# Performance work log

Measured on AMD Instinct MI355X. Metric: run time of the kernel, lower is better.

The kernel has to match this reference:

```python
import jax, jax.numpy as jnp
import numpy as np

INPUT, HIDDEN, OUTPUT = 512, 1024, 512
B, T = 64, 512


def setup_inputs() -> dict:
    key = jax.random.key(0)
    ks = jax.random.split(key, 10)
    s_ih = (2.0 / (INPUT + HIDDEN)) ** 0.5
    s_hh = (2.0 / (INPUT + HIDDEN)) ** 0.5
    s_hy = (2.0 / (HIDDEN + OUTPUT)) ** 0.5
    inp = {
        "x": jax.random.normal(ks[0], (B, T, INPUT), dtype=jnp.float32),
        "W_xi": jax.random.normal(ks[1], (INPUT, HIDDEN), dtype=jnp.float32) * s_ih,
        "W_hi": jax.random.normal(ks[2], (HIDDEN, HIDDEN), dtype=jnp.float32) * s_hh,
        "b_i": jnp.zeros((HIDDEN,), dtype=jnp.float32),
        "W_xf": jax.random.normal(ks[3], (INPUT, HIDDEN), dtype=jnp.float32) * s_ih,
        "W_hf": jax.random.normal(ks[4], (HIDDEN, HIDDEN), dtype=jnp.float32) * s_hh,
        "b_f": jnp.zeros((HIDDEN,), dtype=jnp.float32),
        "W_xo": jax.random.normal(ks[5], (INPUT, HIDDEN), dtype=jnp.float32) * s_ih,
        "W_ho": jax.random.normal(ks[6], (HIDDEN, HIDDEN), dtype=jnp.float32) * s_hh,
        "b_o": jnp.zeros((HIDDEN,), dtype=jnp.float32),
        "W_xc": jax.random.normal(ks[7], (INPUT, HIDDEN), dtype=jnp.float32) * s_ih,
        "W_hc": jax.random.normal(ks[8], (HIDDEN, HIDDEN), dtype=jnp.float32) * s_hh,
        "b_c": jnp.zeros((HIDDEN,), dtype=jnp.float32),
        "W_hy": jax.random.normal(ks[9], (HIDDEN, OUTPUT), dtype=jnp.float32) * s_hy,
        "b_y": jnp.zeros((OUTPUT,), dtype=jnp.float32),
    }
    return inp


def reference(x, W_xi, W_hi, b_i, W_xf, W_hf, b_f, W_xo, W_ho, b_o,
              W_xc, W_hc, b_c, W_hy, b_y):
    Bn, Tn, _ = x.shape
    H = W_hi.shape[0]
    # Precompute input projections for all timesteps (one big GEMM per gate).
    xi = jnp.einsum('bti,ih->bth', x, W_xi) + b_i  # [B,T,H]
    xf = jnp.einsum('bti,ih->bth', x, W_xf) + b_f
    xo = jnp.einsum('bti,ih->bth', x, W_xo) + b_o
    xc = jnp.einsum('bti,ih->bth', x, W_xc) + b_c
    # time-major for scan
    xs = (jnp.swapaxes(xi, 0, 1), jnp.swapaxes(xf, 0, 1),
          jnp.swapaxes(xo, 0, 1), jnp.swapaxes(xc, 0, 1))

    def step(carry, xt):
        h, c = carry
        xi_t, xf_t, xo_t, xc_t = xt
        i_t = jax.nn.sigmoid(xi_t + h @ W_hi)
        f_t = jax.nn.sigmoid(xf_t + h @ W_hf)
        o_t = jax.nn.sigmoid(xo_t + h @ W_ho)
        cand = jnp.tanh(xc_t + h @ W_hc)
        c = f_t * c + i_t * cand
        h = o_t * jnp.tanh(c)
        return (h, c), h

    h0 = jnp.zeros((Bn, H), dtype=x.dtype)
    c0 = jnp.zeros((Bn, H), dtype=x.dtype)
    _, hs = jax.lax.scan(step, (h0, c0), xs)  # hs: [T,B,H]
    # Output projection applied to every step's hidden state.
    ys = jnp.einsum('tbh,ho->tbo', hs, W_hy) + b_y
    return jnp.swapaxes(ys, 0, 1)  # [B,T,O]
```

## Files before the change

kernel.cpp:

```cpp
#include <hip/hip_runtime.h>
#include <hip/hip_bf16.h>
#include <cstdint>

#define B_   64
#define T_   512
#define IN_  512
#define H_   1024
#define O_   512
#define NG   4096
#define KC   1536
#define BT   32768
#define BH   65536
#define NWG  256

#define GLB __attribute__((address_space(1)))
#define LDSAS __attribute__((address_space(3)))

using bs8 = __attribute__((ext_vector_type(8))) short;
using f4  = __attribute__((ext_vector_type(4))) float;
using u32x4 = __attribute__((ext_vector_type(4))) unsigned int;

__device__ __forceinline__ ushort f2bf(float f) {
    union { float f; uint32_t u; } v; v.f = f;
    uint32_t r = v.u + 0x7fffu + ((v.u >> 16) & 1u);
    return (ushort)(r >> 16);
}
__device__ __forceinline__ float sigm(float x) { return 1.f / (1.f + __expf(-x)); }
__device__ __forceinline__ float tanh_(float x) {
    x = fminf(fmaxf(x, -15.f), 15.f);
    float e = __expf(2.f * x);
    return (e - 1.f) / (e + 1.f);
}


__global__ void k_pack_x(const float* __restrict__ x, ushort* __restrict__ xP) {
    const int n8 = BT * IN_ / 8;
    for (int i = blockIdx.x * blockDim.x + threadIdx.x; i < n8; i += gridDim.x * blockDim.x) {
        const int e8 = i & 3, b = (i >> 2) & 63, kk = (i >> 8) & 15, t = i >> 12;
        const float* s = x + ((size_t)b * T_ + t) * IN_ + kk * 32 + e8 * 8;
        f4 v0 = *reinterpret_cast<const f4*>(s);
        f4 v1 = *reinterpret_cast<const f4*>(s + 4);
        uint4 q;
        q.x = (uint32_t)f2bf(v0[0]) | ((uint32_t)f2bf(v0[1]) << 16);
        q.y = (uint32_t)f2bf(v0[2]) | ((uint32_t)f2bf(v0[3]) << 16);
        q.z = (uint32_t)f2bf(v1[0]) | ((uint32_t)f2bf(v1[1]) << 16);
        q.w = (uint32_t)f2bf(v1[2]) | ((uint32_t)f2bf(v1[3]) << 16);
        *reinterpret_cast<uint4*>(xP + ((size_t)t * 16 + kk) * 2048 + b * 32 + e8 * 8) = q;
    }
}

__global__ void k_build_wcT(const float* __restrict__ xi, const float* __restrict__ xf,
                            const float* __restrict__ xo, const float* __restrict__ xc,
                            const float* __restrict__ hi, const float* __restrict__ hf,
                            const float* __restrict__ ho, const float* __restrict__ hc,
                            ushort* __restrict__ dst) {
    const int total = NG * KC;
    for (int i = blockIdx.x * blockDim.x + threadIdx.x; i < total; i += gridDim.x * blockDim.x) {
        int n = i / KC, k = i - n * KC;
        int g = n & 3, h = n >> 2;
        float v;
        if (k < IN_) {
            const float* s = (g == 0) ? xi : ((g == 1) ? xf : ((g == 2) ? xo : xc));
            v = s[(size_t)k * H_ + h];
        } else {
            const float* s = (g == 0) ? hi : ((g == 1) ? hf : ((g == 2) ? ho : hc));
            v = s[(size_t)(k - IN_) * H_ + h];
        }
        dst[i] = f2bf(v);
    }
}

__global__ void k_build_whyT(const float* __restrict__ w, ushort* __restrict__ dst) {
    const int total = O_ * H_;
    for (int i = blockIdx.x * blockDim.x + threadIdx.x; i < total; i += gridDim.x * blockDim.x) {
        int o = i >> 10, k = i & (H_ - 1);
        dst[i] = f2bf(w[(size_t)k * O_ + o]);
    }
}

__global__ void k_build_bias(const float* __restrict__ bi, const float* __restrict__ bff,
                             const float* __restrict__ bo, const float* __restrict__ bc,
                             float* __restrict__ dst) {
    int i = blockIdx.x * blockDim.x + threadIdx.x;
    if (i < NG) {
        int g = i & 3, h = i >> 2;
        dst[i] = (g == 0) ? bi[h] : ((g == 1) ? bff[h] : ((g == 2) ? bo[h] : bc[h]));
    }
}

__global__ void __launch_bounds__(256) __attribute__((amdgpu_waves_per_eu(1, 1)))
k_persist(const ushort* __restrict__ WcT, const ushort* __restrict__ xP,
          ushort* __restrict__ hs, float* __restrict__ cst,
          const float* __restrict__ biasc, uint32_t* __restrict__ flags,
          int t0, int nsteps) {
    __shared__ char Hst[4][32][1024];
    __shared__ ushort hout[64][4];
    const int g = blockIdx.x, tid = threadIdx.x;
    const int lane = tid & 63, w = tid >> 6;
    const int n0 = g * 16;
    const int l15 = lane & 15, lq = lane >> 4;

    bs8 wf[48];
#pragma unroll
    for (int c = 0; c < 48; ++c)
        wf[c] = *reinterpret_cast<const bs8*>(WcT + (size_t)(n0 + l15) * KC + c * 32 + lq * 8);

    const int bmy = w * 16 + l15;
    const int u = g * 4 + lq;
    const f4 bia = *reinterpret_cast<const f4*>(biasc + n0 + lq * 4);
    float creg = (t0 == 0) ? 0.f : cst[(size_t)bmy * H_ + u];

    const int lgo = ((lane >> 3) * 512) + (w * 128) + ((lane & 7) * 16);
    const char* hsb = (const char*)hs;
    const ushort* xb = xP + (size_t)bmy * 32 + lq * 8;
    const int lro = ((l15 >> 1) * 16) + ((l15 & 1) * 8);

    bs8 xv[16];
#pragma unroll
    for (int c = 0; c < 16; ++c)
        xv[c] = *reinterpret_cast<const bs8*>(xb + ((size_t)t0 * 16 + c) * 2048);

    __syncthreads();

    f4 acc[4];
    auto hcons = [&](int c) {
        const char* base = &Hst[w][c][0] + lro;
        union { bs8 v; uint2 p[2]; } uu;
        uu.p[0] = *reinterpret_cast<const uint2*>(base + (lq * 2 + 0) * 128);
        uu.p[1] = *reinterpret_cast<const uint2*>(base + (lq * 2 + 1) * 128);
        acc[c & 3] = __builtin_amdgcn_mfma_f32_16x16x32_bf16(wf[16 + c], uu.v, acc[c & 3], 0, 0, 0);
    };

    for (int s = 0; s < nsteps; ++s) {
        const char* slot = hsb + (size_t)s * 131072 + lgo;
#pragma unroll
        for (int c = 0; c < 32; ++c)
            __builtin_amdgcn_global_load_lds((const GLB uint32_t*)(slot + c * 4096),
                                             (LDSAS uint32_t*)(&Hst[w][c][0]), 16, 0, 0);

#pragma unroll
        for (int c = 0; c < 4; ++c) acc[c] = (f4){0.f, 0.f, 0.f, 0.f};
#pragma unroll
        for (int c = 0; c < 16; ++c)
            acc[c & 3] = __builtin_amdgcn_mfma_f32_16x16x32_bf16(wf[c], xv[c], acc[c & 3], 0, 0, 0);

        asm volatile("s_waitcnt vmcnt(24)" ::: "memory");
        __builtin_amdgcn_sched_barrier(0);
#pragma unroll
        for (int j = 0; j < 8; ++j) hcons(j);
        asm volatile("s_waitcnt vmcnt(16)" ::: "memory");
        __builtin_amdgcn_sched_barrier(0);
#pragma unroll
        for (int j = 8; j < 16; ++j) hcons(j);
        asm volatile("s_waitcnt vmcnt(8)" ::: "memory");
        __builtin_amdgcn_sched_barrier(0);
#pragma unroll
        for (int j = 16; j < 24; ++j) hcons(j);
        asm volatile("s_waitcnt vmcnt(0)" ::: "memory");
        __builtin_amdgcn_sched_barrier(0);
#pragma unroll
        for (int j = 24; j < 32; ++j) hcons(j);

        f4 ssum = (acc[0] + acc[1]) + (acc[2] + acc[3]);

        {
            float pi = ssum[0] + bia[0], pf = ssum[1] + bia[1];
            float po = ssum[2] + bia[2], pc = ssum[3] + bia[3];
            float iv = sigm(pi), fv = sigm(pf), ov = sigm(po), cv = tanh_(pc);
            creg = fv * creg + iv * cv;
            hout[bmy][lq] = f2bf(ov * tanh_(creg));
        }
        __syncthreads();

        if (w == 0) {
            uint2 hv2 = *reinterpret_cast<uint2*>(&hout[lane][0]);
            char* dst = (char*)hs + (size_t)(s + 1) * 131072 + (size_t)g * 512 + lane * 8;
            asm volatile("global_store_dwordx2 %0, %1, off sc0 sc1" :: "v"(dst), "v"(hv2) : "memory");
            asm volatile("s_waitcnt vmcnt(0)" ::: "memory");
            if (tid == 0)
                __hip_atomic_store(&flags[g], (uint32_t)(s + 1),
                                   __ATOMIC_RELAXED, __HIP_MEMORY_SCOPE_AGENT);
        }

        if (s + 1 < nsteps) {
#pragma unroll
            for (int c = 0; c < 16; ++c)
                xv[c] = *reinterpret_cast<const bs8*>(xb + ((size_t)(t0 + s + 1) * 16 + c) * 2048);
            if (w == 0) {
                const uint32_t tgt = (uint32_t)(s + 1);
                const uint32_t* fp = flags + lane * 4;
                for (;;) {
                    u32x4 f;
                    asm volatile("global_load_dwordx4 %0, %1, off sc0 sc1\n\t"
                                 "s_waitcnt vmcnt(0)"
                                 : "=v"(f) : "v"(fp) : "memory");
                    if (__all((int)(f.x >= tgt && f.y >= tgt && f.z >= tgt && f.w >= tgt))) break;
                    __builtin_amdgcn_s_sleep(1);
                }
            }
            __syncthreads();
        }
    }

    cst[(size_t)bmy * H_ + u] = creg;
}

__global__ void __launch_bounds__(64) k_yproj(const ushort* __restrict__ WhyT,
                                              const ushort* __restrict__ hsbase,
                                              const float* __restrict__ by,
                                              float* __restrict__ out, int t_off) {
    const int lane = threadIdx.x;
    const int tloc = blockIdx.x;
    const int o0 = blockIdx.y * 64;
    const int l15 = lane & 15, lq = lane >> 4, lk = lq * 8;
    const int t = t_off + tloc;

    const char* slot = (const char*)(hsbase + (size_t)(tloc + 1) * BH);
    const ushort* apm[4];
#pragma unroll
    for (int m = 0; m < 4; ++m) apm[m] = WhyT + (size_t)(o0 + m * 16 + l15) * H_ + lk;

    f4 acc[4][4] = {};
    for (int kk = 0; kk < 32; ++kk) {
        bs8 a[4], b[4];
#pragma unroll
        for (int m = 0; m < 4; ++m) a[m] = *reinterpret_cast<const bs8*>(apm[m] + kk * 32);
#pragma unroll
        for (int n = 0; n < 4; ++n) {
            const int bb = n * 16 + l15;
            union { bs8 v; uint2 p[2]; } uu;
            uu.p[0] = *reinterpret_cast<const uint2*>(slot + (size_t)(kk * 8 + lq * 2 + 0) * 512 + bb * 8);
            uu.p[1] = *reinterpret_cast<const uint2*>(slot + (size_t)(kk * 8 + lq * 2 + 1) * 512 + bb * 8);
            b[n] = uu.v;
        }
#pragma unroll
        for (int m = 0; m < 4; ++m)
#pragma unroll
            for (int n = 0; n < 4; ++n)
                acc[m][n] = __builtin_amdgcn_mfma_f32_16x16x32_bf16(a[m], b[n], acc[m][n], 0, 0, 0);
    }

#pragma unroll
    for (int m = 0; m < 4; ++m) {
        const int ob = o0 + m * 16 + lq * 4;
        const f4 bb = *reinterpret_cast<const f4*>(by + ob);
#pragma unroll
        for (int n = 0; n < 4; ++n) {
            const int b_ = n * 16 + l15;
            f4 v = acc[m][n] + bb;
            *reinterpret_cast<f4*>(out + ((size_t)b_ * T_ + t) * O_ + ob) = v;
        }
    }
}


extern "C" void kernel_launch(void* const* d_in, const int* in_sizes, int n_in,
                              void* d_out, int out_size, void* d_ws, size_t ws_size,
                              hipStream_t stream) {
    const float* x   = (const float*)d_in[0];
    const float* wxi = (const float*)d_in[1];
    const float* whi = (const float*)d_in[2];
    const float* bi  = (const float*)d_in[3];
    const float* wxf = (const float*)d_in[4];
    const float* whf = (const float*)d_in[5];
    const float* bf_ = (const float*)d_in[6];
    const float* wxo = (const float*)d_in[7];
    const float* who = (const float*)d_in[8];
    const float* bo  = (const float*)d_in[9];
    const float* wxc = (const float*)d_in[10];
    const float* whc = (const float*)d_in[11];
    const float* bc  = (const float*)d_in[12];
    const float* why = (const float*)d_in[13];
    const float* by  = (const float*)d_in[14];
    float* out = (float*)d_out;

    uint8_t* w = (uint8_t*)d_ws;
    ushort*   xP    = (ushort*)  (w);
    ushort*   WcT   = (ushort*)  (w + 33554432);
    ushort*   WhyT  = (ushort*)  (w + 46137344);
    float*    biasc = (float*)   (w + 47185920);
    float*    cst   = (float*)   (w + 47202304);
    uint32_t* flags = (uint32_t*)(w + 47464448);
    ushort*   hs    = (ushort*)  (w + 47468544);
    const size_t NEED_A = 47468544 + (size_t)(T_ + 1) * BH * 2;
    const size_t NEED_B = 47468544 + (size_t)65 * BH * 2;
    if (ws_size < NEED_B) return;
    const bool fullhs = (ws_size >= NEED_A);

    k_pack_x<<<2048, 256, 0, stream>>>(x, xP);
    k_build_wcT<<<4096, 256, 0, stream>>>(wxi, wxf, wxo, wxc, whi, whf, who, whc, WcT);
    k_build_whyT<<<512, 256, 0, stream>>>(why, WhyT);
    k_build_bias<<<16, 256, 0, stream>>>(bi, bf_, bo, bc, biasc);

    hipMemsetAsync(cst, 0, (size_t)BH * 4, stream);
    hipMemsetAsync(hs,  0, (size_t)BH * 2, stream);

    const int nchunk = fullhs ? 1 : 8;
    const int steps  = fullhs ? T_ : 64;
    for (int c = 0; c < nchunk; ++c) {
        const int t0 = c * steps;
        hipMemsetAsync(flags, 0, NWG * 4, stream);
        const ushort* a0 = WcT; const ushort* a1 = xP; ushort* a2 = hs;
        float* a3 = cst; const float* a4 = biasc; uint32_t* a5 = flags;
        int a6 = t0, a7 = steps;
        void* args[8] = {&a0, &a1, &a2, &a3, &a4, &a5, &a6, &a7};
        hipError_t e = hipLaunchCooperativeKernel((const void*)k_persist,
                                                  dim3(NWG), dim3(256), args, 0, stream);
        if (e != hipSuccess) {
            k_persist<<<dim3(NWG), dim3(256), 0, stream>>>(WcT, xP, hs, cst, biasc,
                                                           flags, t0, steps);
        }
        if (!fullhs) {
            k_yproj<<<dim3(64, O_ / 64), 64, 0, stream>>>(WhyT, hs, by, out, t0);
            if (c != nchunk - 1)
                hipMemcpyAsync(hs, hs + (size_t)64 * BH, (size_t)BH * 2,
                               hipMemcpyDeviceToDevice, stream);
        }
    }
    if (fullhs)
        k_yproj<<<dim3(T_, O_ / 64), 64, 0, stream>>>(WhyT, hs, by, out, 0);
}
```

Before: 2.695 ms.

## Split recurrent K across waves and overlap input-projection MFMAs with flag wait

Each wave now owns a quarter of the K-chunks for all 64 batch rows instead of the full K for 16 rows. Per-wave weight registers drop from 48 to 12 fragments, and the partial sums are reduced across waves through an LDS buffer. The input-projection MFMAs for the next step are issued before the flag poll, and the flag store no longer waits for all outstanding loads, so less of that work sits on the serial critical path. In exchange this adds an extra LDS reduction and barrier, and every wave now polls the flags without a trailing block barrier, which risks races on the shared buffers.

```diff
diff --git a/kernel.cpp b/kernel.cpp
--- a/kernel.cpp
+++ b/kernel.cpp
@@ -94,74 +94,91 @@
           const float* __restrict__ biasc, uint32_t* __restrict__ flags,
           int t0, int nsteps) {
     __shared__ char Hst[4][32][1024];
+    __shared__ f4 part[4][4][64];
     __shared__ ushort hout[64][4];
     const int g = blockIdx.x, tid = threadIdx.x;
     const int lane = tid & 63, w = tid >> 6;
     const int n0 = g * 16;
     const int l15 = lane & 15, lq = lane >> 4;
 
-    bs8 wf[48];
-#pragma unroll
-    for (int c = 0; c < 48; ++c)
-        wf[c] = *reinterpret_cast<const bs8*>(WcT + (size_t)(n0 + l15) * KC + c * 32 + lq * 8);
+    bs8 wf[12];
+#pragma unroll
+    for (int i = 0; i < 4; ++i)
+        wf[i] = *reinterpret_cast<const bs8*>(WcT + (size_t)(n0 + l15) * KC + (w + 4 * i) * 32 + lq * 8);
+#pragma unroll
+    for (int i = 0; i < 8; ++i)
+        wf[4 + i] = *reinterpret_cast<const bs8*>(WcT + (size_t)(n0 + l15) * KC + 512 + (w + 4 * i) * 32 + lq * 8);
 
     const int bmy = w * 16 + l15;
     const int u = g * 4 + lq;
     const f4 bia = *reinterpret_cast<const f4*>(biasc + n0 + lq * 4);
     float creg = (t0 == 0) ? 0.f : cst[(size_t)bmy * H_ + u];
 
-    const int lgo = ((lane >> 3) * 512) + (w * 128) + ((lane & 7) * 16);
     const char* hsb = (const char*)hs;
-    const ushort* xb = xP + (size_t)bmy * 32 + lq * 8;
+    const int lsg = ((lane >> 3) << 9) + ((lane & 7) << 4);
     const int lro = ((l15 >> 1) * 16) + ((l15 & 1) * 8);
 
     bs8 xv[16];
 #pragma unroll
-    for (int c = 0; c < 16; ++c)
-        xv[c] = *reinterpret_cast<const bs8*>(xb + ((size_t)t0 * 16 + c) * 2048);
+    for (int i = 0; i < 4; ++i)
+#pragma unroll
+        for (int bt = 0; bt < 4; ++bt)
+            xv[i * 4 + bt] = *reinterpret_cast<const bs8*>(
+                xP + ((size_t)t0 * 16 + (w + 4 * i)) * 2048 + (bt * 16 + l15) * 32 + lq * 8);
+    f4 acc[4];
+#pragma unroll
+    for (int bt = 0; bt < 4; ++bt) acc[bt] = (f4){0.f, 0.f, 0.f, 0.f};
+#pragma unroll
+    for (int i = 0; i < 4; ++i)
+#pragma unroll
+        for (int bt = 0; bt < 4; ++bt)
+            acc[bt] = __builtin_amdgcn_mfma_f32_16x16x32_bf16(wf[i], xv[i * 4 + bt], acc[bt], 0, 0, 0);
 
     __syncthreads();
 
-    f4 acc[4];
-    auto hcons = [&](int c) {
-        const char* base = &Hst[w][c][0] + lro;
+    auto hcons = [&](int i, int bt) {
+        const char* base = &Hst[w][i * 4 + bt][0] + lro;
         union { bs8 v; uint2 p[2]; } uu;
         uu.p[0] = *reinterpret_cast<const uint2*>(base + (lq * 2 + 0) * 128);
         uu.p[1] = *reinterpret_cast<const uint2*>(base + (lq * 2 + 1) * 128);
-        acc[c & 3] = __builtin_amdgcn_mfma_f32_16x16x32_bf16(wf[16 + c], uu.v, acc[c & 3], 0, 0, 0);
+        acc[bt] = __builtin_amdgcn_mfma_f32_16x16x32_bf16(wf[4 + i], uu.v, acc[bt], 0, 0, 0);
     };
 
     for (int s = 0; s < nsteps; ++s) {
-        const char* slot = hsb + (size_t)s * 131072 + lgo;
-#pragma unroll
-        for (int c = 0; c < 32; ++c)
-            __builtin_amdgcn_global_load_lds((const GLB uint32_t*)(slot + c * 4096),
-                                             (LDSAS uint32_t*)(&Hst[w][c][0]), 16, 0, 0);
-
-#pragma unroll
-        for (int c = 0; c < 4; ++c) acc[c] = (f4){0.f, 0.f, 0.f, 0.f};
-#pragma unroll
-        for (int c = 0; c < 16; ++c)
-            acc[c & 3] = __builtin_amdgcn_mfma_f32_16x16x32_bf16(wf[c], xv[c], acc[c & 3], 0, 0, 0);
+        {
+            const char* slot = hsb + (size_t)s * 131072;
+#pragma unroll
+            for (int i = 0; i < 8; ++i) {
+                const int hc = w + 4 * i;
+                const char* csrc = slot + (size_t)hc * 4096 + lsg;
+#pragma unroll
+                for (int bt = 0; bt < 4; ++bt)
+                    __builtin_amdgcn_global_load_lds((const GLB uint32_t*)(csrc + bt * 128),
+                                                     (LDSAS uint32_t*)(&Hst[w][i * 4 + bt][0]), 16, 0, 0);
+            }
+        }
 
         asm volatile("s_waitcnt vmcnt(24)" ::: "memory");
         __builtin_amdgcn_sched_barrier(0);
 #pragma unroll
-        for (int j = 0; j < 8; ++j) hcons(j);
+        for (int i = 0; i < 2; ++i) { hcons(i, 0); hcons(i, 1); hcons(i, 2); hcons(i, 3); }
         asm volatile("s_waitcnt vmcnt(16)" ::: "memory");
         __builtin_amdgcn_sched_barrier(0);
 #pragma unroll
-        for (int j = 8; j < 16; ++j) hcons(j);
+        for (int i = 2; i < 4; ++i) { hcons(i, 0); hcons(i, 1); hcons(i, 2); hcons(i, 3); }
         asm volatile("s_waitcnt vmcnt(8)" ::: "memory");
         __builtin_amdgcn_sched_barrier(0);
 #pragma unroll
-        for (int j = 16; j < 24; ++j) hcons(j);
+        for (int i = 4; i < 6; ++i) { hcons(i, 0); hcons(i, 1); hcons(i, 2); hcons(i, 3); }
         asm volatile("s_waitcnt vmcnt(0)" ::: "memory");
         __builtin_amdgcn_sched_barrier(0);
 #pragma unroll
-        for (int j = 24; j < 32; ++j) hcons(j);
-
-        f4 ssum = (acc[0] + acc[1]) + (acc[2] + acc[3]);
+        for (int i = 6; i < 8; ++i) { hcons(i, 0); hcons(i, 1); hcons(i, 2); hcons(i, 3); }
+
+#pragma unroll
+        for (int bt = 0; bt < 4; ++bt) part[w][bt][lane] = acc[bt];
+        __syncthreads();
+        f4 ssum = (part[0][w][lane] + part[1][w][lane]) + (part[2][w][lane] + part[3][w][lane]);
 
         {
             float pi = ssum[0] + bia[0], pf = ssum[1] + bia[1];
@@ -176,17 +193,29 @@
             uint2 hv2 = *reinterpret_cast<uint2*>(&hout[lane][0]);
             char* dst = (char*)hs + (size_t)(s + 1) * 131072 + (size_t)g * 512 + lane * 8;
             asm volatile("global_store_dwordx2 %0, %1, off sc0 sc1" :: "v"(dst), "v"(hv2) : "memory");
-            asm volatile("s_waitcnt vmcnt(0)" ::: "memory");
-            if (tid == 0)
-                __hip_atomic_store(&flags[g], (uint32_t)(s + 1),
-                                   __ATOMIC_RELAXED, __HIP_MEMORY_SCOPE_AGENT);
         }
 
         if (s + 1 < nsteps) {
 #pragma unroll
-            for (int c = 0; c < 16; ++c)
-                xv[c] = *reinterpret_cast<const bs8*>(xb + ((size_t)(t0 + s + 1) * 16 + c) * 2048);
+            for (int i = 0; i < 4; ++i)
+#pragma unroll
+                for (int bt = 0; bt < 4; ++bt)
+                    xv[i * 4 + bt] = *reinterpret_cast<const bs8*>(
+                        xP + ((size_t)(t0 + s + 1) * 16 + (w + 4 * i)) * 2048 + (bt * 16 + l15) * 32 + lq * 8);
             if (w == 0) {
+                asm volatile("s_waitcnt vmcnt(16)" ::: "memory");
+                if (tid == 0)
+                    __hip_atomic_store(&flags[g], (uint32_t)(s + 1),
+                                       __ATOMIC_RELAXED, __HIP_MEMORY_SCOPE_AGENT);
+            }
+#pragma unroll
+            for (int bt = 0; bt < 4; ++bt) acc[bt] = (f4){0.f, 0.f, 0.f, 0.f};
+#pragma unroll
+            for (int i = 0; i < 4; ++i)
+#pragma unroll
+                for (int bt = 0; bt < 4; ++bt)
+                    acc[bt] = __builtin_amdgcn_mfma_f32_16x16x32_bf16(wf[i], xv[i * 4 + bt], acc[bt], 0, 0, 0);
+            {
                 const uint32_t tgt = (uint32_t)(s + 1);
                 const uint32_t* fp = flags + lane * 4;
                 for (;;) {
@@ -198,7 +227,13 @@
                     __builtin_amdgcn_s_sleep(1);
                 }
             }
-            __syncthreads();
+        } else {
+            if (w == 0) {
+                asm volatile("s_waitcnt vmcnt(0)" ::: "memory");
+                if (tid == 0)
+                    __hip_atomic_store(&flags[g], (uint32_t)(s + 1),
+                                       __ATOMIC_RELAXED, __HIP_MEMORY_SCOPE_AGENT);
+            }
         }
     }
 
```

Result: slower. 3.510 ms (+30.3%).
